# Kernel optimization log

Hardware: AMD Instinct MI355X
Metric: run time of the kernel (lower is better)

## Reference

```python
import jax, jax.numpy as jnp
import numpy as np

B, N, E = 8, 1000, 16000
HIST, PRED = 8, 12
IN_DIM = 14          # pm25(1) + met features(13)
HID_GAT, HEADS = 256, 8
GNN_OUT = 13
HID = 64             # GRU hidden (self.hid_dim = 64 in source)


def setup_inputs() -> dict:
    key = jax.random.key(0)
    ks = jax.random.split(key, 20)
    p = lambda k, shp, s=0.05: jax.random.normal(k, shp, dtype=jnp.float32) * s
    return {
        "pm25_hist": jax.random.normal(ks[0], (B, HIST, N, 1), dtype=jnp.float32),
        "feature": jax.random.normal(ks[1], (B, HIST + PRED, N, IN_DIM - 1), dtype=jnp.float32),
        "edge_index": jax.random.randint(ks[2], (2, E), 0, N),
        "gat1_W": p(ks[3], (IN_DIM, HEADS * HID_GAT)),
        "gat1_att_src": p(ks[4], (HEADS, HID_GAT)),
        "gat1_att_dst": p(ks[5], (HEADS, HID_GAT)),
        "gat1_b": p(ks[6], (HEADS * HID_GAT,)),
        "gat2_W": p(ks[7], (HEADS * HID_GAT, GNN_OUT)),
        "gat2_att_src": p(ks[8], (1, GNN_OUT)),
        "gat2_att_dst": p(ks[9], (1, GNN_OUT)),
        "gat2_b": p(ks[10], (GNN_OUT,)),
        "gru_W_ih": p(ks[11], (3 * HID, IN_DIM + GNN_OUT)),
        "gru_W_hh": p(ks[12], (3 * HID, HID)),
        "gru_b_ih": p(ks[13], (3 * HID,)),
        "gru_b_hh": p(ks[14], (3 * HID,)),
        "fc_out_W": p(ks[15], (HID, 1)),
        "fc_out_b": p(ks[16], (1,)),
    }


def _gat_conv(x, W, a_src, a_dst, b, src, dst, concat):
    # Single-graph GATConv (PyG semantics, eval mode: dropout disabled).
    # x: [N, F_in]; src/dst: [E'] (self-loops already appended)
    H, D = a_src.shape
    h = (x @ W).reshape(N, H, D)                       # [N, H, D]
    e = jax.nn.leaky_relu(
        (h * a_src).sum(-1)[src] + (h * a_dst).sum(-1)[dst], 0.2
    )                                                  # [E', H]
    # segment softmax over incoming edges of each dst node
    m = jax.ops.segment_max(e, dst, num_segments=N)
    ex = jnp.exp(e - m[dst])
    alpha = ex / jax.ops.segment_sum(ex, dst, num_segments=N)[dst]
    out = jax.ops.segment_sum(alpha[:, :, None] * h[src], dst, num_segments=N)  # [N, H, D]
    return (out.reshape(N, H * D) + b) if concat else (out.mean(1) + b)


def reference(pm25_hist, feature, edge_index,
              gat1_W, gat1_att_src, gat1_att_dst, gat1_b,
              gat2_W, gat2_att_src, gat2_att_dst, gat2_b,
              gru_W_ih, gru_W_hh, gru_b_ih, gru_b_hh,
              fc_out_W, fc_out_b):
    # add self-loops (PyG GATConv default)
    loop = jnp.arange(N)
    src = jnp.concatenate([edge_index[0], loop])
    dst = jnp.concatenate([edge_index[1], loop])

    def gnn(x):  # x: [N, IN_DIM] -> [N, GNN_OUT]
        h = jax.nn.elu(_gat_conv(x, gat1_W, gat1_att_src, gat1_att_dst, gat1_b, src, dst, True))
        return _gat_conv(h, gat2_W, gat2_att_src, gat2_att_dst, gat2_b, src, dst, False)

    gnn_b = jax.vmap(gnn)

    def gru(x, h):  # torch.nn.GRUCell math
        i_r, i_z, i_n = jnp.split(x @ gru_W_ih.T + gru_b_ih, 3, axis=-1)
        h_r, h_z, h_n = jnp.split(h @ gru_W_hh.T + gru_b_hh, 3, axis=-1)
        r = jax.nn.sigmoid(i_r + h_r)
        z = jax.nn.sigmoid(i_z + h_z)
        n = jnp.tanh(i_n + r * h_n)
        return (1.0 - z) * n + z * h

    feats = jnp.moveaxis(feature[:, HIST:HIST + PRED], 1, 0)  # [PRED, B, N, 13]

    def step(carry, f_t):
        hn, xn = carry
        x = jnp.concatenate([xn, f_t], axis=-1)               # [B, N, IN_DIM]
        g = gnn_b(x)                                          # [B, N, GNN_OUT]
        gx = jnp.concatenate([g, x], axis=-1).reshape(B * N, IN_DIM + GNN_OUT)
        hn = gru(gx, hn)                                      # [B*N, HID]
        xn = hn.reshape(B, N, HID) @ fc_out_W + fc_out_b      # [B, N, 1]
        return (hn, xn), xn

    h0 = jnp.zeros((B * N, HID), jnp.float32)
    xn0 = pm25_hist[:, -1]                                    # [B, N, 1]
    _, preds = jax.lax.scan(step, (h0, xn0), feats)
    return jnp.moveaxis(preds, 0, 1)                          # [B, PRED, N, 1]
```

## Files before the change

kernel.cpp:

```cpp
#include <hip/hip_runtime.h>
#include <hip/hip_bf16.h>
#include <math.h>

#define BB 8
#define NN 1000
#define EE 16000
#define ETOT 17000
#define TPRED 12
#define FEAT 13
#define INDIM 14
#define HEADS 8
#define HG 256
#define C1 2048
#define GO 13
#define HID 64

typedef unsigned int  uint32;
typedef unsigned short ushort16;
typedef uint32 uvec4 __attribute__((ext_vector_type(4)));
typedef __fp16 hf2 __attribute__((ext_vector_type(2)));

union U32H2 { uint32 u; hf2 h; };
__device__ __forceinline__ hf2 u2h(uint32 u){ U32H2 c; c.u=u; return c.h; }
__device__ __forceinline__ uint32 h2u(hf2 h){ U32H2 c; c.h=h; return c.u; }

#if __has_builtin(__builtin_amdgcn_fdot2)
__device__ __forceinline__ float FDOT2(hf2 a, hf2 b, float c){
    return __builtin_amdgcn_fdot2(a, b, c, false);
}
#else
__device__ __forceinline__ float FDOT2(hf2 a, hf2 b, float c){
    return c + (float)a.x*(float)b.x + (float)a.y*(float)b.y;
}
#endif

__device__ __forceinline__ float lrelu(float v){ return v > 0.f ? v : 0.2f*v; }

__device__ __forceinline__ ushort16 f2bf(float f){
    union { float f; uint32 u; } v; v.f = f;
    uint32 r = v.u + 0x7FFFu + ((v.u >> 16) & 1u);
    return (ushort16)(r >> 16);
}
__device__ __forceinline__ uint32 pack2(float lo, float hi){
    return (uint32)f2bf(lo) | ((uint32)f2bf(hi) << 16);
}
__device__ __forceinline__ void cvt2(uint32 u, float& lo, float& hi){
    union { uint32 u; float f; } a, b;
    a.u = u << 16; b.u = u & 0xFFFF0000u;
    lo = a.f; hi = b.f;
}
__device__ __forceinline__ uint32 pkh(float lo, float hi){
    hf2 h; h.x = (__fp16)lo; h.y = (__fp16)hi; return h2u(h);
}

__global__ void k_prep(const float* W1, const float* a1s, const float* a1d,
                       const float* W2, const float* a2s, const float* a2d,
                       const float* Wih, const float* Whh,
                       float* Wsrc, float* Wdst, uint32* w1pk, uint32* w2pk,
                       uint32* WihP, uint32* WhhP){
    __shared__ float rs[4], rd[4];
    int bid = blockIdx.x, tid = threadIdx.x;
    if (bid < 112){
        int k = bid >> 3, h = bid & 7;
        float wv = W1[k*C1 + h*HG + tid];
        float ps = wv * a1s[h*HG + tid];
        float pd = wv * a1d[h*HG + tid];
        #pragma unroll
        for (int m=1;m<64;m<<=1){ ps += __shfl_xor(ps,m); pd += __shfl_xor(pd,m); }
        int w = tid>>6;
        if ((tid&63)==0){ rs[w]=ps; rd[w]=pd; }
        __syncthreads();
        if (tid==0){
            Wsrc[k*8+h] = rs[0]+rs[1]+rs[2]+rs[3];
            Wdst[k*8+h] = rd[0]+rd[1]+rd[2]+rd[3];
        }
    } else if (bid < 176){
        int i = (bid-112)*256 + tid;
        int c = i >> 3, kk = i & 7;
        float lo = (kk < 7) ? W1[(2*kk)*C1 + c]   : 0.f;
        float hi = (kk < 7) ? W1[(2*kk+1)*C1 + c] : 0.f;
        w1pk[i] = h2u(__builtin_amdgcn_cvt_pkrtz(lo, hi));
    } else if (bid < 180){
        int m = (bid-176)*256 + tid;
        if (m < C1/2){
            int c0 = 2*m, c1 = 2*m+1;
            float colA[16], colB[16];
            float ssA=0.f, ddA=0.f, ssB=0.f, ddB=0.f;
            #pragma unroll
            for (int j=0;j<GO;j++){
                float wA = W2[c0*GO+j], wB = W2[c1*GO+j];
                colA[j]=wA; colB[j]=wB;
                ssA += wA*a2s[j]; ddA += wA*a2d[j];
                ssB += wB*a2s[j]; ddB += wB*a2d[j];
            }
            colA[13]=ssA; colA[14]=ddA; colA[15]=0.f;
            colB[13]=ssB; colB[14]=ddB; colB[15]=0.f;
            #pragma unroll
            for (int j=0;j<16;j++)
                w2pk[m*16+j] = h2u(__builtin_amdgcn_cvt_pkrtz(colA[j], colB[j]));
        }
    } else {
        int i = (bid-180)*256 + tid;
        if (i < 192*14){
            int rr = i/14, c2 = i - rr*14;
            float lo = Wih[rr*27 + 2*c2];
            float hi = (2*c2+1 < 27) ? Wih[rr*27 + 2*c2 + 1] : 0.f;
            WihP[i] = pkh(lo, hi);
        }
        if (i < 192*32){
            int rr = i>>5, j2 = i&31;
            WhhP[i] = pkh(Whh[rr*64 + 2*j2], Whh[rr*64 + 2*j2 + 1]);
        }
    }
}

__global__ void k_init(const float* pm25, const float* feat,
                       const float* Wsrc, const float* Wdst,
                       float* hn, float* xn, int* count,
                       float* ssrc, float* sdst, uint32* xpk){
    int i = blockIdx.x*blockDim.x + threadIdx.x;
    if (i < BB*NN*HID) hn[i] = 0.f;
    if (i < NN) count[i] = 0;
    if (i < BB*NN){
        int b = i/NN, n = i%NN;
        float x[INDIM];
        x[0] = pm25[(b*8 + 7)*NN + n];
        xn[i] = x[0];
        const float* fp = feat + ((size_t)(b*20 + 8)*NN + n)*FEAT;
        #pragma unroll
        for (int k=0;k<FEAT;k++) x[k+1] = fp[k];
        #pragma unroll
        for (int h=0;h<8;h++){
            float ss=0.f, dd=0.f;
            #pragma unroll
            for (int k=0;k<INDIM;k++){ ss += x[k]*Wsrc[k*8+h]; dd += x[k]*Wdst[k*8+h]; }
            ssrc[i*8+h] = ss; sdst[i*8+h] = dd;
        }
        #pragma unroll
        for (int p=0;p<7;p++) xpk[i*8+p] = pack2(x[2*p], x[2*p+1]);
        xpk[i*8+7] = 0u;
    }
}

__global__ void k_count(const int* ei, int* count){
    int e = blockIdx.x*blockDim.x + threadIdx.x;
    if (e < ETOT){
        int dst = (e<EE) ? ei[EE+e] : (e-EE);
        atomicAdd(&count[dst], 1);
    }
}

__global__ void k_scan(const int* count, int* offs, int* cursor){
    __shared__ int s[1024];
    int tid = threadIdx.x;
    int myc = (tid<NN) ? count[tid] : 0;
    s[tid] = myc;
    __syncthreads();
    for (int d=1; d<1024; d<<=1){
        int v = (tid>=d) ? s[tid-d] : 0;
        __syncthreads();
        s[tid] += v;
        __syncthreads();
    }
    if (tid<NN){
        int off = s[tid] - myc;
        offs[tid] = off; cursor[tid] = off;
    }
    if (tid==NN-1) offs[NN] = s[tid];
}

__global__ void k_fill(const int* ei, int* cursor, int* csr_src){
    int e = blockIdx.x*blockDim.x + threadIdx.x;
    if (e < ETOT){
        int src = (e<EE) ? ei[e]    : (e-EE);
        int dst = (e<EE) ? ei[EE+e] : (e-EE);
        int pos = atomicAdd(&cursor[dst], 1);
        csr_src[pos] = src;
    }
}


__global__ __launch_bounds__(64) void k_agg14(const uint32* xpk, const float* ssrc,
        const float* sdst, const int* offs, const int* csr, uint32* aggP){
    int lane = threadIdx.x;
    int blk = blockIdx.x;
    int b = blk & 7, dstn = blk >> 3;
    int bn = b*NN + dstn;
    int base = offs[dstn], deg = offs[dstn+1]-base;
    int slot = lane >> 3, h = lane & 7;
    float sdd = sdst[bn*8 + h];
    float m = -1e30f, d = 0.f;
    float acc[14];
    #pragma unroll
    for (int k=0;k<14;k++) acc[k]=0.f;
    for (int i=slot;i<deg;i+=8){
        int s = csr[base+i];
        float sc = lrelu(ssrc[(b*NN+s)*8+h]+sdd);
        float w;
        if (sc > m){
            float e = __expf(m - sc);
            d *= e;
            #pragma unroll
            for (int k=0;k<14;k++) acc[k] *= e;
            m = sc; w = 1.f;
        } else {
            w = __expf(sc - m);
        }
        d += w;
        const uint32* xp = xpk + (size_t)(b*NN+s)*8;
        #pragma unroll
        for (int p=0;p<7;p++){
            float x0,x1; cvt2(xp[p],x0,x1);
            acc[2*p]   += w*x0;
            acc[2*p+1] += w*x1;
        }
    }
    #pragma unroll
    for (int st=8; st<64; st<<=1){
        float m2 = __shfl_xor(m, st);
        float d2 = __shfl_xor(d, st);
        float mn = fmaxf(m, m2);
        float e1 = __expf(m - mn), e2 = __expf(m2 - mn);
        d = d*e1 + d2*e2;
        #pragma unroll
        for (int k=0;k<14;k++){
            float a2 = __shfl_xor(acc[k], st);
            acc[k] = acc[k]*e1 + a2*e2;
        }
        m = mn;
    }
    if (slot==0){
        float rden = 1.f/d;
        uint32* ag = aggP + (size_t)bn*64 + h*8;
        #pragma unroll
        for (int p=0;p<7;p++)
            ag[p] = h2u(__builtin_amdgcn_cvt_pkrtz(acc[2*p]*rden, acc[2*p+1]*rden));
        ag[7] = 0u;
    }
}

__global__ __launch_bounds__(256,1) void k_expand(const uint32* aggP, const uint32* w1pk,
        const uint32* w2pk, const float* b1, float* h2o, float* s2s, float* s2d){
    int tid = threadIdx.x;
    int hh = tid >> 5;
    uint32 w1r[64];
    #pragma unroll
    for (int q=0;q<16;q++){
        uvec4 u = *(const uvec4*)(w1pk + tid*64 + 4*q);
        w1r[4*q]=u.x; w1r[4*q+1]=u.y; w1r[4*q+2]=u.z; w1r[4*q+3]=u.w;
    }
    uint32 w2r[64];
    #pragma unroll
    for (int q=0;q<16;q++){
        uvec4 u = *(const uvec4*)(w2pk + tid*64 + 4*q);
        w2r[4*q]=u.x; w2r[4*q+1]=u.y; w2r[4*q+2]=u.z; w2r[4*q+3]=u.w;
    }
    float b1r[8];
    #pragma unroll
    for (int j=0;j<8;j++) b1r[j] = b1[8*tid+j];
    __shared__ float sred[256*17];
    __shared__ float red2[64];
    for (int idx = blockIdx.x; idx < BB*NN; idx += gridDim.x){
        const uvec4* ap = (const uvec4*)(aggP + (size_t)idx*64 + hh*8);
        uvec4 u0 = ap[0], u1 = ap[1];
        hf2 agh[7];
        agh[0]=u2h(u0.x); agh[1]=u2h(u0.y); agh[2]=u2h(u0.z); agh[3]=u2h(u0.w);
        agh[4]=u2h(u1.x); agh[5]=u2h(u1.y); agh[6]=u2h(u1.z);
        float v[8];
        #pragma unroll
        for (int j=0;j<8;j++){
            float s = b1r[j];
            #pragma unroll
            for (int kk=0;kk<7;kk++) s = FDOT2(agh[kk], u2h(w1r[j*8+kk]), s);
            v[j] = s > 0.f ? s : __expf(s) - 1.f;
        }
        hf2 vp[4];
        #pragma unroll
        for (int q=0;q<4;q++) vp[q] = __builtin_amdgcn_cvt_pkrtz(v[2*q], v[2*q+1]);
        #pragma unroll
        for (int j=0;j<16;j++){
            float s = 0.f;
            #pragma unroll
            for (int q=0;q<4;q++) s = FDOT2(vp[q], u2h(w2r[q*16+j]), s);
            sred[tid*17 + j] = s;
        }
        __syncthreads();
        int j = tid & 15, g = tid >> 4;
        float s = 0.f;
        #pragma unroll
        for (int i=0;i<16;i++) s += sred[(g + 16*i)*17 + j];
        s += __shfl_xor(s, 16);
        s += __shfl_xor(s, 32);
        int lane = tid & 63, w = tid >> 6;
        if (lane < 16) red2[w*16 + lane] = s;
        __syncthreads();
        if (tid < 15){
            float r = red2[tid] + red2[16+tid] + red2[32+tid] + red2[48+tid];
            if (tid < GO)      h2o[idx*GO + tid] = r;
            else if (tid==13)  s2s[idx] = r;
            else               s2d[idx] = r;
        }
        __syncthreads();
    }
}

__global__ __launch_bounds__(64,2) void k_tail(int t, int last,
        const float* feat, const int* offs, const int* csr,
        const float* h2, const float* s2src, const float* s2dst, const float* b2,
        const uint32* WihP, const uint32* WhhP, const float* bih, const float* bhh,
        const float* fcw, const float* fcb, const float* Wsrc, const float* Wdst,
        float* hn, float* xn, float* out,
        float* ssrc, float* sdst, uint32* xpk){
    int lane = threadIdx.x;
    uint32 wih0[14], wih1[14], wih2[14];
    #pragma unroll
    for (int q=0;q<14;q++){
        wih0[q]=WihP[lane*14+q];
        wih1[q]=WihP[(64+lane)*14+q];
        wih2[q]=WihP[(128+lane)*14+q];
    }
    uint32 whh0[32], whh1[32], whh2[32];
    #pragma unroll
    for (int q=0;q<32;q++){
        whh0[q]=WhhP[lane*32+q];
        whh1[q]=WhhP[(64+lane)*32+q];
        whh2[q]=WhhP[(128+lane)*32+q];
    }
    float bi0=bih[lane], bi1=bih[64+lane], bi2=bih[128+lane];
    float bh0=bhh[lane], bh1=bhh[64+lane], bh2=bhh[128+lane];
    float fw = fcw[lane], fb = fcb[0];
    float b2r[GO];
    #pragma unroll
    for (int c=0;c<GO;c++) b2r[c] = b2[c];
    __shared__ uint32 hsP[32];
    for (int r=0;r<4;r++){
        int bn = blockIdx.x*4 + r;
        int b = bn/NN, n = bn - b*NN;
        int base = offs[n], deg = offs[n+1]-base;
        float sdd = s2dst[bn];
        float m = -1e30f, d = 0.f;
        float acc[GO];
        #pragma unroll
        for (int c=0;c<GO;c++) acc[c]=0.f;
        for (int e=lane;e<deg;e+=64){
            int s = csr[base+e];
            float sc = lrelu(s2src[b*NN+s] + sdd);
            float w;
            if (sc > m){
                float ee = __expf(m - sc);
                d *= ee;
                #pragma unroll
                for (int c=0;c<GO;c++) acc[c] *= ee;
                m = sc; w = 1.f;
            } else {
                w = __expf(sc - m);
            }
            d += w;
            const float* hr2 = h2 + (size_t)(b*NN+s)*GO;
            #pragma unroll
            for (int c=0;c<GO;c++) acc[c] += w*hr2[c];
        }
        #pragma unroll
        for (int st=1; st<64; st<<=1){
            float m2 = __shfl_xor(m, st);
            float d2 = __shfl_xor(d, st);
            float mn = fmaxf(m, m2);
            float e1 = __expf(m - mn), e2 = __expf(m2 - mn);
            d = d*e1 + d2*e2;
            #pragma unroll
            for (int c=0;c<GO;c++){
                float a2 = __shfl_xor(acc[c], st);
                acc[c] = acc[c]*e1 + a2*e2;
            }
            m = mn;
        }
        float rdv = 1.f / d;
        float xnv = xn[bn];
        const float* fp = feat + ((size_t)(b*20 + 8 + t)*NN + n)*FEAT;
        float ft[FEAT];
        #pragma unroll
        for (int k=0;k<FEAT;k++) ft[k] = fp[k];
        hf2 gx[14];
        #pragma unroll
        for (int p=0;p<6;p++)
            gx[p] = u2h(pkh(acc[2*p]*rdv+b2r[2*p], acc[2*p+1]*rdv+b2r[2*p+1]));
        gx[6] = u2h(pkh(acc[12]*rdv+b2r[12], xnv));
        #pragma unroll
        for (int p=0;p<6;p++)
            gx[7+p] = u2h(pkh(ft[2*p], ft[2*p+1]));
        gx[13] = u2h(pkh(ft[12], 0.f));
        float hold = hn[bn*HID + lane];
        if (lane<32) hsP[lane] = pkh(hn[bn*HID + 2*lane], hn[bn*HID + 2*lane + 1]);
        __syncthreads();
        float ir = bi0, iz = bi1, inn = bi2;
        #pragma unroll
        for (int c2=0;c2<14;c2++){
            ir  = FDOT2(gx[c2], u2h(wih0[c2]), ir);
            iz  = FDOT2(gx[c2], u2h(wih1[c2]), iz);
            inn = FDOT2(gx[c2], u2h(wih2[c2]), inn);
        }
        float hr = bh0, hz = bh1, hnv = bh2;
        #pragma unroll
        for (int j2=0;j2<32;j2++){
            hf2 hv = u2h(hsP[j2]);
            hr  = FDOT2(hv, u2h(whh0[j2]), hr);
            hz  = FDOT2(hv, u2h(whh1[j2]), hz);
            hnv = FDOT2(hv, u2h(whh2[j2]), hnv);
        }
        float rg = 1.f/(1.f+__expf(-(ir+hr)));
        float zg = 1.f/(1.f+__expf(-(iz+hz)));
        float nv = tanhf(inn + rg*hnv);
        float hnew = (1.f - zg)*nv + zg*hold;
        hn[bn*HID+lane] = hnew;
        float xv = hnew * fw;
        #pragma unroll
        for (int mm=1;mm<64;mm<<=1) xv += __shfl_xor(xv,mm);
        float res = xv + fb;
        if (lane==0){
            xn[bn] = res;
            out[(b*TPRED + t)*NN + n] = res;
        }
        if (!last){
            const float* fp2 = feat + ((size_t)(b*20 + 9 + t)*NN + n)*FEAT;
            if (lane < 16){
                int h = lane & 7;
                const float* Wa = (lane<8) ? Wsrc : Wdst;
                float s = res * Wa[h];
                #pragma unroll
                for (int k=1;k<14;k++) s += fp2[k-1]*Wa[k*8+h];
                if (lane<8) ssrc[bn*8+h] = s; else sdst[bn*8+h] = s;
            } else if (lane < 23){
                int p = lane - 16;
                float lo = (p==0) ? res : fp2[2*p-1];
                float hi = fp2[2*p];
                xpk[bn*8+p] = pack2(lo, hi);
            } else if (lane == 23){
                xpk[bn*8+7] = 0u;
            }
        }
        __syncthreads();
    }
}


extern "C" void kernel_launch(void* const* d_in, const int* in_sizes, int n_in,
                              void* d_out, int out_size, void* d_ws, size_t ws_size,
                              hipStream_t stream){
    const float* pm25 = (const float*)d_in[0];
    const float* feat = (const float*)d_in[1];
    const int*   ei   = (const int*)  d_in[2];
    const float* W1   = (const float*)d_in[3];
    const float* a1s  = (const float*)d_in[4];
    const float* a1d  = (const float*)d_in[5];
    const float* b1   = (const float*)d_in[6];
    const float* W2   = (const float*)d_in[7];
    const float* a2s  = (const float*)d_in[8];
    const float* a2d  = (const float*)d_in[9];
    const float* b2   = (const float*)d_in[10];
    const float* Wih  = (const float*)d_in[11];
    const float* Whh  = (const float*)d_in[12];
    const float* bih  = (const float*)d_in[13];
    const float* bhh  = (const float*)d_in[14];
    const float* fcw  = (const float*)d_in[15];
    const float* fcb  = (const float*)d_in[16];
    float* out = (float*)d_out;

    float* f = (float*)d_ws;
    size_t o = 0;
    float* ssrc1 = f+o; o += (size_t)BB*NN*8;
    float* sdst1 = f+o; o += (size_t)BB*NN*8;
    uint32* aggP = (uint32*)(f+o); o += (size_t)BB*NN*64;
    float* h2    = f+o; o += (size_t)BB*NN*GO + 8;
    float* s2s   = f+o; o += (size_t)BB*NN;
    float* s2d   = f+o; o += (size_t)BB*NN;
    float* hn    = f+o; o += (size_t)BB*NN*HID;
    float* xn    = f+o; o += (size_t)BB*NN;
    float* Wsrc  = f+o; o += INDIM*8;
    float* Wdst  = f+o; o += INDIM*8;
    uint32* xpk  = (uint32*)(f+o); o += (size_t)BB*NN*8;
    uint32* w1pk = (uint32*)(f+o); o += (size_t)C1*8;
    uint32* w2pk = (uint32*)(f+o); o += (size_t)(C1/2)*16;
    uint32* WihP = (uint32*)(f+o); o += 192*14;
    uint32* WhhP = (uint32*)(f+o); o += 192*32;
    int* ibase  = (int*)(f+o);
    int* count  = ibase;
    int* cursor = ibase + NN;
    int* offs   = ibase + 2*NN;
    int* csr    = ibase + 2*NN + NN + 1;

    k_prep  <<<204, 256,0,stream>>>(W1, a1s, a1d, W2, a2s, a2d, Wih, Whh,
                                    Wsrc, Wdst, w1pk, w2pk, WihP, WhhP);
    k_init  <<<2000,256,0,stream>>>(pm25, feat, Wsrc, Wdst, hn, xn, count,
                                    ssrc1, sdst1, xpk);
    k_count <<<67,  256,0,stream>>>(ei, count);
    k_scan  <<<1,  1024,0,stream>>>(count, offs, cursor);
    k_fill  <<<67,  256,0,stream>>>(ei, cursor, csr);

    for (int t=0; t<TPRED; t++){
        k_agg14 <<<8000, 64,0,stream>>>(xpk, ssrc1, sdst1, offs, csr, aggP);
        k_expand<<<512, 256,0,stream>>>(aggP, w1pk, w2pk, b1, h2, s2s, s2d);
        k_tail  <<<2000, 64,0,stream>>>(t, (t==TPRED-1)?1:0, feat, offs, csr,
                                        h2, s2s, s2d, b2,
                                        WihP, WhhP, bih, bhh, fcw, fcb, Wsrc, Wdst,
                                        hn, xn, out, ssrc1, sdst1, xpk);
    }
}
```

Before: 779.0 us.

## Simplify softmax cross-lane merges and process two nodes per k_expand iteration

```diff
diff --git a/kernel.cpp b/kernel.cpp
--- a/kernel.cpp
+++ b/kernel.cpp
@@ -215,19 +215,20 @@
             acc[2*p+1] += w*x1;
         }
     }
-    #pragma unroll
-    for (int st=8; st<64; st<<=1){
-        float m2 = __shfl_xor(m, st);
-        float d2 = __shfl_xor(d, st);
-        float mn = fmaxf(m, m2);
-        float e1 = __expf(m - mn), e2 = __expf(m2 - mn);
-        d = d*e1 + d2*e2;
-        #pragma unroll
-        for (int k=0;k<14;k++){
-            float a2 = __shfl_xor(acc[k], st);
-            acc[k] = acc[k]*e1 + a2*e2;
-        }
-        m = mn;
+    float mloc = m;
+    m = fmaxf(m, __shfl_xor(m,8));
+    m = fmaxf(m, __shfl_xor(m,16));
+    m = fmaxf(m, __shfl_xor(m,32));
+    float wr = __expf(mloc - m);
+    d *= wr;
+    #pragma unroll
+    for (int k=0;k<14;k++) acc[k] *= wr;
+    d += __shfl_xor(d,8); d += __shfl_xor(d,16); d += __shfl_xor(d,32);
+    #pragma unroll
+    for (int k=0;k<14;k++){
+        acc[k] += __shfl_xor(acc[k],8);
+        acc[k] += __shfl_xor(acc[k],16);
+        acc[k] += __shfl_xor(acc[k],32);
     }
     if (slot==0){
         float rden = 1.f/d;
@@ -258,47 +259,86 @@
     float b1r[8];
     #pragma unroll
     for (int j=0;j<8;j++) b1r[j] = b1[8*tid+j];
-    __shared__ float sred[256*17];
-    __shared__ float red2[64];
-    for (int idx = blockIdx.x; idx < BB*NN; idx += gridDim.x){
-        const uvec4* ap = (const uvec4*)(aggP + (size_t)idx*64 + hh*8);
-        uvec4 u0 = ap[0], u1 = ap[1];
-        hf2 agh[7];
-        agh[0]=u2h(u0.x); agh[1]=u2h(u0.y); agh[2]=u2h(u0.z); agh[3]=u2h(u0.w);
-        agh[4]=u2h(u1.x); agh[5]=u2h(u1.y); agh[6]=u2h(u1.z);
-        float v[8];
-        #pragma unroll
-        for (int j=0;j<8;j++){
-            float s = b1r[j];
-            #pragma unroll
-            for (int kk=0;kk<7;kk++) s = FDOT2(agh[kk], u2h(w1r[j*8+kk]), s);
-            v[j] = s > 0.f ? s : __expf(s) - 1.f;
-        }
-        hf2 vp[4];
-        #pragma unroll
-        for (int q=0;q<4;q++) vp[q] = __builtin_amdgcn_cvt_pkrtz(v[2*q], v[2*q+1]);
-        #pragma unroll
-        for (int j=0;j<16;j++){
-            float s = 0.f;
-            #pragma unroll
-            for (int q=0;q<4;q++) s = FDOT2(vp[q], u2h(w2r[q*16+j]), s);
-            sred[tid*17 + j] = s;
+    __shared__ float sred0[256*17], sred1[256*17];
+    __shared__ float red2a[64], red2b[64];
+    for (int r = 0; r < 8; ++r){
+        int idx0 = blockIdx.x + r*1024;
+        int idx1 = idx0 + 512;
+        bool ok1 = (idx1 < BB*NN);
+        {
+            const uvec4* ap = (const uvec4*)(aggP + (size_t)idx0*64 + hh*8);
+            uvec4 u0 = ap[0], u1 = ap[1];
+            hf2 agh[7];
+            agh[0]=u2h(u0.x); agh[1]=u2h(u0.y); agh[2]=u2h(u0.z); agh[3]=u2h(u0.w);
+            agh[4]=u2h(u1.x); agh[5]=u2h(u1.y); agh[6]=u2h(u1.z);
+            float v[8];
+            #pragma unroll
+            for (int j=0;j<8;j++){
+                float s = b1r[j];
+                #pragma unroll
+                for (int kk=0;kk<7;kk++) s = FDOT2(agh[kk], u2h(w1r[j*8+kk]), s);
+                v[j] = s > 0.f ? s : __expf(s) - 1.f;
+            }
+            hf2 vp[4];
+            #pragma unroll
+            for (int q=0;q<4;q++) vp[q] = __builtin_amdgcn_cvt_pkrtz(v[2*q], v[2*q+1]);
+            #pragma unroll
+            for (int j=0;j<16;j++){
+                float s = 0.f;
+                #pragma unroll
+                for (int q=0;q<4;q++) s = FDOT2(vp[q], u2h(w2r[q*16+j]), s);
+                sred0[tid*17 + j] = s;
+            }
+        }
+        if (ok1){
+            const uvec4* ap = (const uvec4*)(aggP + (size_t)idx1*64 + hh*8);
+            uvec4 u0 = ap[0], u1 = ap[1];
+            hf2 agh[7];
+            agh[0]=u2h(u0.x); agh[1]=u2h(u0.y); agh[2]=u2h(u0.z); agh[3]=u2h(u0.w);
+            agh[4]=u2h(u1.x); agh[5]=u2h(u1.y); agh[6]=u2h(u1.z);
+            float v[8];
+            #pragma unroll
+            for (int j=0;j<8;j++){
+                float s = b1r[j];
+                #pragma unroll
+                for (int kk=0;kk<7;kk++) s = FDOT2(agh[kk], u2h(w1r[j*8+kk]), s);
+                v[j] = s > 0.f ? s : __expf(s) - 1.f;
+            }
+            hf2 vp[4];
+            #pragma unroll
+            for (int q=0;q<4;q++) vp[q] = __builtin_amdgcn_cvt_pkrtz(v[2*q], v[2*q+1]);
+            #pragma unroll
+            for (int j=0;j<16;j++){
+                float s = 0.f;
+                #pragma unroll
+                for (int q=0;q<4;q++) s = FDOT2(vp[q], u2h(w2r[q*16+j]), s);
+                sred1[tid*17 + j] = s;
+            }
         }
         __syncthreads();
         int j = tid & 15, g = tid >> 4;
-        float s = 0.f;
-        #pragma unroll
-        for (int i=0;i<16;i++) s += sred[(g + 16*i)*17 + j];
-        s += __shfl_xor(s, 16);
-        s += __shfl_xor(s, 32);
+        float s0 = 0.f, s1 = 0.f;
+        #pragma unroll
+        for (int i=0;i<16;i++){
+            s0 += sred0[(g + 16*i)*17 + j];
+            s1 += sred1[(g + 16*i)*17 + j];
+        }
+        s0 += __shfl_xor(s0, 16); s0 += __shfl_xor(s0, 32);
+        s1 += __shfl_xor(s1, 16); s1 += __shfl_xor(s1, 32);
         int lane = tid & 63, w = tid >> 6;
-        if (lane < 16) red2[w*16 + lane] = s;
+        if (lane < 16){ red2a[w*16 + lane] = s0; red2b[w*16 + lane] = s1; }
         __syncthreads();
         if (tid < 15){
-            float r = red2[tid] + red2[16+tid] + red2[32+tid] + red2[48+tid];
-            if (tid < GO)      h2o[idx*GO + tid] = r;
-            else if (tid==13)  s2s[idx] = r;
-            else               s2d[idx] = r;
+            float rv = red2a[tid] + red2a[16+tid] + red2a[32+tid] + red2a[48+tid];
+            if (tid < GO)      h2o[idx0*GO + tid] = rv;
+            else if (tid==13)  s2s[idx0] = rv;
+            else               s2d[idx0] = rv;
+        } else if (tid >= 16 && tid < 31 && ok1){
+            int c = tid - 16;
+            float rv = red2b[c] + red2b[16+c] + red2b[32+c] + red2b[48+c];
+            if (c < GO)        h2o[idx1*GO + c] = rv;
+            else if (c==13)    s2s[idx1] = rv;
+            else               s2d[idx1] = rv;
         }
         __syncthreads();
     }
@@ -360,19 +400,18 @@
             #pragma unroll
             for (int c=0;c<GO;c++) acc[c] += w*hr2[c];
         }
+        float mloc = m;
+        #pragma unroll
+        for (int st=1; st<64; st<<=1) m = fmaxf(m, __shfl_xor(m, st));
+        float wr = __expf(mloc - m);
+        d *= wr;
+        #pragma unroll
+        for (int c=0;c<GO;c++) acc[c] *= wr;
         #pragma unroll
         for (int st=1; st<64; st<<=1){
-            float m2 = __shfl_xor(m, st);
-            float d2 = __shfl_xor(d, st);
-            float mn = fmaxf(m, m2);
-            float e1 = __expf(m - mn), e2 = __expf(m2 - mn);
-            d = d*e1 + d2*e2;
-            #pragma unroll
-            for (int c=0;c<GO;c++){
-                float a2 = __shfl_xor(acc[c], st);
-                acc[c] = acc[c]*e1 + a2*e2;
-            }
-            m = mn;
+            d += __shfl_xor(d, st);
+            #pragma unroll
+            for (int c=0;c<GO;c++) acc[c] += __shfl_xor(acc[c], st);
         }
         float rdv = 1.f / d;
         float xnv = xn[bn];
```

New measurement: 798.9 us. +2.5%, slower.
